# Kernel optimization log

Hardware: AMD Instinct MI355X
Metric: run time of the kernel (lower is better)

The kernel has to match this reference:

```python
import jax, jax.numpy as jnp
import numpy as np

N_GROUPS = 8
N_TOPK_GROUP = 4
TOPK = 8
ROUTED_SCALE = 2.5


def setup_inputs() -> dict:
    key = jax.random.key(0)
    k1, k2, k3 = jax.random.split(key, 3)
    T, D, E = 8192, 7168, 256
    x = jax.random.normal(k1, (T, D), dtype=jnp.float32)
    weight = jax.random.normal(k2, (E, D), dtype=jnp.float32) * 0.02
    bias = jax.random.normal(k3, (E,), dtype=jnp.float32) * 0.02
    return {"x": x, "weight": weight, "bias": bias}


def reference(x, weight, bias):
    T = x.shape[0]
    # gate projection + sigmoid -> routing scores [T, E]
    scores = jax.nn.sigmoid(jnp.einsum("td,ed->te", x, weight))
    original_scores = scores
    s = scores + bias
    # grouped top-k routing: [T, G, E/G]
    sg = s.reshape(T, N_GROUPS, -1)
    # group score = sum of top-2 expert scores within each group
    group_scores = jax.lax.top_k(sg, 2)[0].sum(axis=-1)        # [T, G]
    _, gidx = jax.lax.top_k(group_scores, N_TOPK_GROUP)        # [T, n_topk_group]
    keep = jnp.zeros((T, N_GROUPS), dtype=bool)
    keep = keep.at[jnp.arange(T)[:, None], gidx].set(True)
    sg = jnp.where(keep[:, :, None], sg, -jnp.inf)
    s = sg.reshape(T, -1)
    # per-token top-k experts over surviving groups
    _, indices = jax.lax.top_k(s, TOPK)                        # [T, topk]
    weights = jnp.take_along_axis(original_scores, indices, axis=1)
    weights = weights / weights.sum(axis=-1, keepdims=True) * ROUTED_SCALE
    return weights.astype(x.dtype), indices
```

## Files before the change

### kernel.cpp

```cpp
#include <hip/hip_runtime.h>
#include <hip/hip_bf16.h>
#include <math.h>


typedef _Float16 f16x8 __attribute__((ext_vector_type(8)));
typedef float    f32x4 __attribute__((ext_vector_type(4)));

__device__ __forceinline__ void glds16(const void* g, void* l) {
  __builtin_amdgcn_global_load_lds(
      (const __attribute__((address_space(1))) void*)g,
      (__attribute__((address_space(3))) void*)l, 16, 0, 0);
}

__device__ __forceinline__ unsigned short f2h(float f) {
  _Float16 h = (_Float16)f;
  return __builtin_bit_cast(unsigned short, h);
}
__device__ __forceinline__ float h2f(unsigned short b) {
  return (float)__builtin_bit_cast(_Float16, b);
}

__device__ __forceinline__ int swz(int gi, int row) {
  return gi ^ (row & 3) ^ ((row >> 2) & 3);
}

__global__ __launch_bounds__(256) void convert_w(
    const float* __restrict__ W,
    unsigned short* __restrict__ Whi, unsigned short* __restrict__ Wlo)
{
  const int e = blockIdx.x;
  const int t = threadIdx.x;
  if (t >= 224) return;
  const float* src = W + (size_t)e * 7168 + t * 32;
  const size_t tbase = (size_t)t * 8192 + (size_t)e * 32;
  #pragma unroll
  for (int g = 0; g < 4; ++g) {
    unsigned int hw[4], lw[4];
    #pragma unroll
    for (int p = 0; p < 4; ++p) {
      float f0 = src[g * 8 + 2 * p] * 64.0f;
      float f1 = src[g * 8 + 2 * p + 1] * 64.0f;
      unsigned short h0 = f2h(f0), h1 = f2h(f1);
      unsigned short l0 = f2h((f0 - h2f(h0)) * 2048.0f);
      unsigned short l1 = f2h((f1 - h2f(h1)) * 2048.0f);
      hw[p] = (unsigned)h0 | ((unsigned)h1 << 16);
      lw[p] = (unsigned)l0 | ((unsigned)l1 << 16);
    }
    const size_t base = tbase + (size_t)(swz(g, e) * 8);
    *(uint4*)(Whi + base) = make_uint4(hw[0], hw[1], hw[2], hw[3]);
    *(uint4*)(Wlo + base) = make_uint4(lw[0], lw[1], lw[2], lw[3]);
  }
}

#define BUF_SZ   40960
#define O_ALO    4096
#define O_BH     8192
#define O_BL     24576

__global__ __launch_bounds__(256, 2) void gate_gemm(
    const float* __restrict__ X,
    const unsigned short* __restrict__ Whi,
    const unsigned short* __restrict__ Wlo,
    float* __restrict__ Spart, int D, int TILES, int KS)
{
  __shared__ char lds[81920];

  const int bid = blockIdx.x;
  const int ks = bid % KS;
  const int bm = bid / KS;
  const int tid = threadIdx.x, lane = tid & 63, wid = tid >> 6;
  const int wn = wid;
  const int TM = bm * 64;
  const int k0base = ks * TILES * 32;

  const int srow = tid >> 2, sg = tid & 3;
  const float* xsrc = X + (size_t)(TM + srow) * D + k0base + sg * 8;
  const int aw = srow * 64 + swz(sg, srow) * 16;

  const unsigned short* wh_tile = Whi + (size_t)(ks * TILES) * 8192;
  const unsigned short* wl_tile = Wlo + (size_t)(ks * TILES) * 8192;

  f32x4 acc1[4][4], acc2[4][4];
  #pragma unroll
  for (int m = 0; m < 4; ++m)
    #pragma unroll
    for (int n = 0; n < 4; ++n) { acc1[m][n] = (f32x4)0.0f; acc2[m][n] = (f32x4)0.0f; }

  int aro[4], bro[4];
  const int gi = lane >> 4;
  #pragma unroll
  for (int m = 0; m < 4; ++m) {
    const int row = m * 16 + (lane & 15);
    aro[m] = row * 64 + swz(gi, row) * 16;
  }
  #pragma unroll
  for (int n = 0; n < 4; ++n) {
    const int row = wn * 64 + n * 16 + (lane & 15);
    bro[n] = row * 64 + swz(gi, row) * 16;
  }

  float4 pa0, pa1, pb0, pb1;
  {
    #pragma unroll
    for (int i = 0; i < 4; ++i) {
      const int c = wid * 4 + i;
      glds16(wh_tile + c * 512 + lane * 8, lds + O_BH + c * 1024);
      glds16(wl_tile + c * 512 + lane * 8, lds + O_BL + c * 1024);
    }
    __builtin_amdgcn_sched_barrier(0);
    float4 a0 = *(const float4*)(xsrc);
    float4 a1 = *(const float4*)(xsrc + 4);
    float ff[8] = {a0.x, a0.y, a0.z, a0.w, a1.x, a1.y, a1.z, a1.w};
    unsigned int hw[4], lw[4];
    #pragma unroll
    for (int q = 0; q < 4; ++q) {
      float f0 = ff[2 * q], f1 = ff[2 * q + 1];
      unsigned short h0 = f2h(f0), h1 = f2h(f1);
      unsigned short l0 = f2h((f0 - h2f(h0)) * 2048.0f);
      unsigned short l1 = f2h((f1 - h2f(h1)) * 2048.0f);
      hw[q] = (unsigned)h0 | ((unsigned)h1 << 16);
      lw[q] = (unsigned)l0 | ((unsigned)l1 << 16);
    }
    *(uint4*)(lds + aw)         = make_uint4(hw[0], hw[1], hw[2], hw[3]);
    *(uint4*)(lds + O_ALO + aw) = make_uint4(lw[0], lw[1], lw[2], lw[3]);
    const int s1 = (TILES > 1) ? 1 : 0;
    pa0 = *(const float4*)(xsrc + (size_t)s1 * 32);
    pa1 = *(const float4*)(xsrc + (size_t)s1 * 32 + 4);
    __builtin_amdgcn_sched_barrier(0);
  }
  asm volatile("s_waitcnt vmcnt(2) lgkmcnt(0)" ::: "memory");
  __builtin_amdgcn_sched_barrier(0);
  __builtin_amdgcn_s_barrier();

  int cur = 0;
  for (int s = 0; s < TILES; ++s) {
    const int nxt = cur ^ 1;
    char* base_c = lds + cur * BUF_SZ;
    char* base_n = lds + nxt * BUF_SZ;
    const bool stage_next = (s + 1 < TILES);

    if (stage_next) {
      const unsigned short* wh = wh_tile + (size_t)(s + 1) * 8192;
      const unsigned short* wl = wl_tile + (size_t)(s + 1) * 8192;
      #pragma unroll
      for (int i = 0; i < 4; ++i) {
        const int c = wid * 4 + i;
        glds16(wh + c * 512 + lane * 8, base_n + O_BH + c * 1024);
        glds16(wl + c * 512 + lane * 8, base_n + O_BL + c * 1024);
      }
    }
    __builtin_amdgcn_sched_barrier(0);

    {
      int sn = s + 2; if (sn > TILES - 1) sn = TILES - 1;
      pb0 = *(const float4*)(xsrc + (size_t)sn * 32);
      pb1 = *(const float4*)(xsrc + (size_t)sn * 32 + 4);
    }
    __builtin_amdgcn_sched_barrier(0);

    {
      const char* Ahi = base_c;         const char* Alo = base_c + O_ALO;
      const char* Bh  = base_c + O_BH;  const char* Bl  = base_c + O_BL;
      f16x8 ah[4], al[4], bh[4], bl[4];
      #pragma unroll
      for (int m = 0; m < 4; ++m) {
        ah[m] = *(const f16x8*)(Ahi + aro[m]);
        al[m] = *(const f16x8*)(Alo + aro[m]);
      }
      #pragma unroll
      for (int n = 0; n < 4; ++n) {
        bh[n] = *(const f16x8*)(Bh + bro[n]);
        bl[n] = *(const f16x8*)(Bl + bro[n]);
      }
      __builtin_amdgcn_s_setprio(1);
      #pragma unroll
      for (int m = 0; m < 4; ++m)
        #pragma unroll
        for (int n = 0; n < 4; ++n) {
          acc1[m][n] = __builtin_amdgcn_mfma_f32_16x16x32_f16(ah[m], bh[n], acc1[m][n], 0, 0, 0);
          acc2[m][n] = __builtin_amdgcn_mfma_f32_16x16x32_f16(ah[m], bl[n], acc2[m][n], 0, 0, 0);
          acc2[m][n] = __builtin_amdgcn_mfma_f32_16x16x32_f16(al[m], bh[n], acc2[m][n], 0, 0, 0);
        }
      __builtin_amdgcn_s_setprio(0);
    }

    if (stage_next) {
      float ff[8] = {pa0.x, pa0.y, pa0.z, pa0.w, pa1.x, pa1.y, pa1.z, pa1.w};
      unsigned int hw[4], lw[4];
      #pragma unroll
      for (int q = 0; q < 4; ++q) {
        float f0 = ff[2 * q], f1 = ff[2 * q + 1];
        unsigned short h0 = f2h(f0), h1 = f2h(f1);
        unsigned short l0 = f2h((f0 - h2f(h0)) * 2048.0f);
        unsigned short l1 = f2h((f1 - h2f(h1)) * 2048.0f);
        hw[q] = (unsigned)h0 | ((unsigned)h1 << 16);
        lw[q] = (unsigned)l0 | ((unsigned)l1 << 16);
      }
      *(uint4*)(base_n + aw)         = make_uint4(hw[0], hw[1], hw[2], hw[3]);
      *(uint4*)(base_n + O_ALO + aw) = make_uint4(lw[0], lw[1], lw[2], lw[3]);
    }
    pa0 = pb0; pa1 = pb1;

    asm volatile("s_waitcnt vmcnt(2) lgkmcnt(0)" ::: "memory");
    __builtin_amdgcn_sched_barrier(0);
    __builtin_amdgcn_s_barrier();

    cur = nxt;
  }

  float* Sp = Spart + (size_t)ks * 8192 * 256;
  #pragma unroll
  for (int m = 0; m < 4; ++m)
    #pragma unroll
    for (int n = 0; n < 4; ++n)
      #pragma unroll
      for (int r = 0; r < 4; ++r) {
        const int t = TM + m * 16 + (lane >> 4) * 4 + r;
        const int e = wn * 64 + n * 16 + (lane & 15);
        Sp[(size_t)t * 256 + e] =
            (acc1[m][n][r] + acc2[m][n][r] * (1.0f / 2048.0f)) * (1.0f / 64.0f);
      }
}

__global__ __launch_bounds__(256) void gate_routing(
    const float* __restrict__ Spart, int KS,
    const float* __restrict__ bias,
    float* __restrict__ outw, float* __restrict__ outi, int T)
{
  const int lane = threadIdx.x & 63;
  const int wave = threadIdx.x >> 6;
  const int t = blockIdx.x * 4 + wave;
  if (t >= T) return;

  double l[4] = {0.0, 0.0, 0.0, 0.0};
  for (int ks = 0; ks < KS; ++ks) {
    float4 p = *(const float4*)(Spart + (size_t)ks * T * 256
                                + (size_t)t * 256 + lane * 4);
    l[0] += (double)p.x; l[1] += (double)p.y;
    l[2] += (double)p.z; l[3] += (double)p.w;
  }

  float4 bi = *(const float4*)(bias + lane * 4);
  float orig[4], s[4];
  #pragma unroll
  for (int u = 0; u < 4; ++u)
    orig[u] = 1.0f / (1.0f + expf(-(float)l[u]));
  s[0] = orig[0] + bi.x; s[1] = orig[1] + bi.y;
  s[2] = orig[2] + bi.z; s[3] = orig[3] + bi.w;

  float m1 = -INFINITY, m2 = -INFINITY;
  #pragma unroll
  for (int u = 0; u < 4; ++u) {
    float v = s[u];
    if (v > m1) { m2 = m1; m1 = v; }
    else if (v > m2) { m2 = v; }
  }
  #pragma unroll
  for (int off = 1; off < 8; off <<= 1) {
    float o1 = __shfl_xor(m1, off, 64);
    float o2 = __shfl_xor(m2, off, 64);
    if (o1 > m1) { m2 = fmaxf(m1, o2); m1 = o1; }
    else         { m2 = fmaxf(m2, o1); }
  }
  const float gscore = m1 + m2;

  const int g = lane >> 3;
  int rank = 0;
  #pragma unroll
  for (int j = 0; j < 8; ++j) {
    float gs = __shfl(gscore, j * 8, 64);
    rank += (gs > gscore || (gs == gscore && j < g)) ? 1 : 0;
  }
  if (rank >= 4) { s[0] = s[1] = s[2] = s[3] = -INFINITY; }

  float wsum = 0.0f, sel_w = 0.0f;
  int sel_i = 0;
  #pragma unroll
  for (int it = 0; it < 8; ++it) {
    float bv = s[0]; int bu = 0;
    #pragma unroll
    for (int u = 1; u < 4; ++u)
      if (s[u] > bv) { bv = s[u]; bu = u; }
    float v = bv;
    int ix = lane * 4 + bu;
    float og = orig[bu];
    #pragma unroll
    for (int off = 1; off < 64; off <<= 1) {
      float ov  = __shfl_xor(v,  off, 64);
      int   oix = __shfl_xor(ix, off, 64);
      float oog = __shfl_xor(og, off, 64);
      if (ov > v || (ov == v && oix < ix)) { v = ov; ix = oix; og = oog; }
    }
    if (lane == it) { sel_w = og; sel_i = ix; }
    wsum += og;
    if ((ix >> 2) == lane) s[ix & 3] = -INFINITY;
  }

  if (lane < 8) {
    outw[(size_t)t * 8 + lane] = sel_w / wsum * 2.5f;
    outi[(size_t)t * 8 + lane] = (float)sel_i;
  }
}

extern "C" void kernel_launch(void* const* d_in, const int* in_sizes, int n_in,
                              void* d_out, int out_size, void* d_ws, size_t ws_size,
                              hipStream_t stream) {
  const float* x = (const float*)d_in[0];
  const float* w = (const float*)d_in[1];
  const float* b = (const float*)d_in[2];
  const int E = in_sizes[2];
  const int D = in_sizes[1] / E;
  const int T = in_sizes[0] / D;

  unsigned short* Whi = (unsigned short*)d_ws;
  unsigned short* Wlo = (unsigned short*)((char*)d_ws + (4u << 20));
  float* Spart = (float*)((char*)d_ws + (8u << 20));

  const size_t per_part = (size_t)T * E * 4;
  int KS = 2;
  if (ws_size >= (8u << 20) + 8 * per_part) KS = 8;
  else if (ws_size >= (8u << 20) + 4 * per_part) KS = 4;
  const int TILES = D / (32 * KS);

  float* outw = (float*)d_out;
  float* outi = outw + (size_t)T * 8;

  convert_w<<<E, 256, 0, stream>>>(w, Whi, Wlo);
  gate_gemm<<<KS * (T / 64), 256, 0, stream>>>(x, Whi, Wlo, Spart, D, TILES, KS);
  gate_routing<<<(T + 3) / 4, 256, 0, stream>>>(Spart, KS, b, outw, outi, T);
}
```

Before: 137.3 us.

## Enlarge GEMM block tile to 128 rows with 8 waves and triple-buffered weights

The gate GEMM block now covers 128 token rows with 512 threads arranged as 2x4 waves, so each staged weight tile in LDS serves twice as many rows and weight traffic per output drops. Weight tiles are prefetched two stages ahead through a three-slot LDS ring, and the first two tiles are loaded in the prologue, to hide global-to-LDS latency. LDS use rises to 144 KB per block, so only one block fits per CU. The fixed vmcnt(6) wait may not fully cover the last iteration, where no new weight loads are issued, which risks a late-tile race.

```diff
diff --git a/kernel.cpp b/kernel.cpp
--- a/kernel.cpp
+++ b/kernel.cpp
@@ -52,25 +52,25 @@
   }
 }
 
-#define BUF_SZ   40960
-#define O_ALO    4096
-#define O_BH     8192
-#define O_BL     24576
-
-__global__ __launch_bounds__(256, 2) void gate_gemm(
+#define BUF_SZ   49152
+#define O_ALO    8192
+#define O_BH     16384
+#define O_BL     32768
+
+__global__ __launch_bounds__(512, 2) void gate_gemm(
     const float* __restrict__ X,
     const unsigned short* __restrict__ Whi,
     const unsigned short* __restrict__ Wlo,
     float* __restrict__ Spart, int D, int TILES, int KS)
 {
-  __shared__ char lds[81920];
+  __shared__ char lds[147456];
 
   const int bid = blockIdx.x;
   const int ks = bid % KS;
   const int bm = bid / KS;
   const int tid = threadIdx.x, lane = tid & 63, wid = tid >> 6;
-  const int wn = wid;
-  const int TM = bm * 64;
+  const int wm = wid >> 2, wn = wid & 3;
+  const int TM = bm * 128;
   const int k0base = ks * TILES * 32;
 
   const int srow = tid >> 2, sg = tid & 3;
@@ -90,7 +90,7 @@
   const int gi = lane >> 4;
   #pragma unroll
   for (int m = 0; m < 4; ++m) {
-    const int row = m * 16 + (lane & 15);
+    const int row = wm * 64 + m * 16 + (lane & 15);
     aro[m] = row * 64 + swz(gi, row) * 16;
   }
   #pragma unroll
@@ -101,15 +101,27 @@
 
   float4 pa0, pa1, pb0, pb1;
   {
-    #pragma unroll
-    for (int i = 0; i < 4; ++i) {
-      const int c = wid * 4 + i;
+    float4 a0 = *(const float4*)(xsrc);
+    float4 a1 = *(const float4*)(xsrc + 4);
+    #pragma unroll
+    for (int i = 0; i < 2; ++i) {
+      const int c = wid * 2 + i;
       glds16(wh_tile + c * 512 + lane * 8, lds + O_BH + c * 1024);
       glds16(wl_tile + c * 512 + lane * 8, lds + O_BL + c * 1024);
     }
-    __builtin_amdgcn_sched_barrier(0);
-    float4 a0 = *(const float4*)(xsrc);
-    float4 a1 = *(const float4*)(xsrc + 4);
+    if (TILES > 1) {
+      #pragma unroll
+      for (int i = 0; i < 2; ++i) {
+        const int c = wid * 2 + i;
+        glds16(wh_tile + 8192 + c * 512 + lane * 8, lds + BUF_SZ + O_BH + c * 1024);
+        glds16(wl_tile + 8192 + c * 512 + lane * 8, lds + BUF_SZ + O_BL + c * 1024);
+      }
+    }
+    __builtin_amdgcn_sched_barrier(0);
+    const int s1 = (TILES > 1) ? 1 : 0;
+    pa0 = *(const float4*)(xsrc + (size_t)s1 * 32);
+    pa1 = *(const float4*)(xsrc + (size_t)s1 * 32 + 4);
+    __builtin_amdgcn_sched_barrier(0);
     float ff[8] = {a0.x, a0.y, a0.z, a0.w, a1.x, a1.y, a1.z, a1.w};
     unsigned int hw[4], lw[4];
     #pragma unroll
@@ -123,30 +135,25 @@
     }
     *(uint4*)(lds + aw)         = make_uint4(hw[0], hw[1], hw[2], hw[3]);
     *(uint4*)(lds + O_ALO + aw) = make_uint4(lw[0], lw[1], lw[2], lw[3]);
-    const int s1 = (TILES > 1) ? 1 : 0;
-    pa0 = *(const float4*)(xsrc + (size_t)s1 * 32);
-    pa1 = *(const float4*)(xsrc + (size_t)s1 * 32 + 4);
-    __builtin_amdgcn_sched_barrier(0);
-  }
-  asm volatile("s_waitcnt vmcnt(2) lgkmcnt(0)" ::: "memory");
+    __builtin_amdgcn_sched_barrier(0);
+  }
+  asm volatile("s_waitcnt vmcnt(6) lgkmcnt(0)" ::: "memory");
   __builtin_amdgcn_sched_barrier(0);
   __builtin_amdgcn_s_barrier();
 
-  int cur = 0;
   for (int s = 0; s < TILES; ++s) {
-    const int nxt = cur ^ 1;
-    char* base_c = lds + cur * BUF_SZ;
-    char* base_n = lds + nxt * BUF_SZ;
-    const bool stage_next = (s + 1 < TILES);
-
-    if (stage_next) {
-      const unsigned short* wh = wh_tile + (size_t)(s + 1) * 8192;
-      const unsigned short* wl = wl_tile + (size_t)(s + 1) * 8192;
-      #pragma unroll
-      for (int i = 0; i < 4; ++i) {
-        const int c = wid * 4 + i;
-        glds16(wh + c * 512 + lane * 8, base_n + O_BH + c * 1024);
-        glds16(wl + c * 512 + lane * 8, base_n + O_BL + c * 1024);
+    char* base_c  = lds + (s % 3) * BUF_SZ;
+    char* base_n1 = lds + ((s + 1) % 3) * BUF_SZ;
+    char* base_n2 = lds + ((s + 2) % 3) * BUF_SZ;
+
+    if (s + 2 < TILES) {
+      const unsigned short* wh = wh_tile + (size_t)(s + 2) * 8192;
+      const unsigned short* wl = wl_tile + (size_t)(s + 2) * 8192;
+      #pragma unroll
+      for (int i = 0; i < 2; ++i) {
+        const int c = wid * 2 + i;
+        glds16(wh + c * 512 + lane * 8, base_n2 + O_BH + c * 1024);
+        glds16(wl + c * 512 + lane * 8, base_n2 + O_BL + c * 1024);
       }
     }
     __builtin_amdgcn_sched_barrier(0);
@@ -184,7 +191,7 @@
       __builtin_amdgcn_s_setprio(0);
     }
 
-    if (stage_next) {
+    if (s + 1 < TILES) {
       float ff[8] = {pa0.x, pa0.y, pa0.z, pa0.w, pa1.x, pa1.y, pa1.z, pa1.w};
       unsigned int hw[4], lw[4];
       #pragma unroll
@@ -196,16 +203,14 @@
         hw[q] = (unsigned)h0 | ((unsigned)h1 << 16);
         lw[q] = (unsigned)l0 | ((unsigned)l1 << 16);
       }
-      *(uint4*)(base_n + aw)         = make_uint4(hw[0], hw[1], hw[2], hw[3]);
-      *(uint4*)(base_n + O_ALO + aw) = make_uint4(lw[0], lw[1], lw[2], lw[3]);
+      *(uint4*)(base_n1 + aw)         = make_uint4(hw[0], hw[1], hw[2], hw[3]);
+      *(uint4*)(base_n1 + O_ALO + aw) = make_uint4(lw[0], lw[1], lw[2], lw[3]);
     }
     pa0 = pb0; pa1 = pb1;
 
-    asm volatile("s_waitcnt vmcnt(2) lgkmcnt(0)" ::: "memory");
+    asm volatile("s_waitcnt vmcnt(6) lgkmcnt(0)" ::: "memory");
     __builtin_amdgcn_sched_barrier(0);
     __builtin_amdgcn_s_barrier();
-
-    cur = nxt;
   }
 
   float* Sp = Spart + (size_t)ks * 8192 * 256;
@@ -215,7 +220,7 @@
     for (int n = 0; n < 4; ++n)
       #pragma unroll
       for (int r = 0; r < 4; ++r) {
-        const int t = TM + m * 16 + (lane >> 4) * 4 + r;
+        const int t = TM + wm * 64 + m * 16 + (lane >> 4) * 4 + r;
         const int e = wn * 64 + n * 16 + (lane & 15);
         Sp[(size_t)t * 256 + e] =
             (acc1[m][n][r] + acc2[m][n][r] * (1.0f / 2048.0f)) * (1.0f / 64.0f);
@@ -326,6 +331,6 @@
   float* outi = outw + (size_t)T * 8;
 
   convert_w<<<E, 256, 0, stream>>>(w, Whi, Wlo);
-  gate_gemm<<<KS * (T / 64), 256, 0, stream>>>(x, Whi, Wlo, Spart, D, TILES, KS);
+  gate_gemm<<<KS * (T / 128), 512, 0, stream>>>(x, Whi, Wlo, Spart, D, TILES, KS);
   gate_routing<<<(T + 3) / 4, 256, 0, stream>>>(Spart, KS, b, outw, outi, T);
 }
```

Result: faster. 134.5 us (-2.0%).
